# Optimization experiments

Hardware: AMD Instinct MI355X
Metric: run time of the kernel (lower is better)

Reference implementation:

```python
import jax, jax.numpy as jnp
import numpy as np

N_NODES = 100000
H_FEATS = 128
N_TRIPLETS = 500000


def setup_inputs() -> dict:
    key = jax.random.key(0)
    k_h, k_t, k_w1, k_b1, k_w2, k_b2 = jax.random.split(key, 6)
    h = jax.random.normal(k_h, (N_NODES, H_FEATS), dtype=jnp.float32)
    triplets = jax.random.randint(k_t, (N_TRIPLETS, 3), 0, N_NODES, dtype=jnp.int64)
    # nn.Linear weights: [out, in]
    W1_w = jax.random.normal(k_w1, (H_FEATS, 3 * H_FEATS), dtype=jnp.float32) * 0.05
    W1_b = jax.random.normal(k_b1, (H_FEATS,), dtype=jnp.float32) * 0.05
    W2_w = jax.random.normal(k_w2, (2, H_FEATS), dtype=jnp.float32) * 0.05
    W2_b = jax.random.normal(k_b2, (2,), dtype=jnp.float32) * 0.05
    return {"h": h, "triplets": triplets, "W1_w": W1_w, "W1_b": W1_b,
            "W2_w": W2_w, "W2_b": W2_b}


def reference(h, triplets, W1_w, W1_b, W2_w, W2_b):
    # gather: [T, 3, H] -> [T, 3*H]
    T = triplets.shape[0]
    emb = h[triplets].reshape(T, 3 * H_FEATS)
    hid = jax.nn.relu(emb @ W1_w.T + W1_b)   # [T, H]
    out = hid @ W2_w.T + W2_b                # [T, 2]
    return out
```

## Files before the change

### kernel.cpp

```cpp
#include <hip/hip_runtime.h>

typedef __bf16 bf16x8 __attribute__((ext_vector_type(8)));
typedef float f32x4 __attribute__((ext_vector_type(4)));

__device__ __forceinline__ unsigned short f2bf(float x) {
  union { float f; unsigned int i; } u; u.f = x;
  return (unsigned short)((u.i + 0x7FFFu + ((u.i >> 16) & 1u)) >> 16);
}
__device__ __forceinline__ float bf2f(unsigned short b) {
  union { unsigned int i; float f; } u; u.i = ((unsigned int)b) << 16;
  return u.f;
}
__device__ __forceinline__ bf16x8 cvt8(float4 a, float4 b) {
  union { unsigned short u[8]; bf16x8 v; } r;
  r.u[0] = f2bf(a.x); r.u[1] = f2bf(a.y); r.u[2] = f2bf(a.z); r.u[3] = f2bf(a.w);
  r.u[4] = f2bf(b.x); r.u[5] = f2bf(b.y); r.u[6] = f2bf(b.z); r.u[7] = f2bf(b.w);
  return r.v;
}

__global__ void pack_w1_kernel(const float* __restrict__ W1w, uint4* __restrict__ wp) {
  int fid = blockIdx.x * 256 + threadIdx.x;
  int kk = fid / 1536;
  int rem = fid - kk * 1536;
  int nf = rem >> 6;
  int ln = rem & 63;
  int ng = nf * 16 + (ln & 15);
  int c = ng & 127;
  int jp = ng >> 7;
  int k0 = kk * 32 + (ln >> 4) * 8;
  const float* src = W1w + (size_t)c * 384 + jp * 128 + k0;
  float4 a = *(const float4*)src;
  float4 b = *(const float4*)(src + 4);
  union { unsigned short u[8]; uint4 v; } r;
  r.u[0] = f2bf(a.x); r.u[1] = f2bf(a.y); r.u[2] = f2bf(a.z); r.u[3] = f2bf(a.w);
  r.u[4] = f2bf(b.x); r.u[5] = f2bf(b.y); r.u[6] = f2bf(b.z); r.u[7] = f2bf(b.w);
  wp[fid] = r.v;
}

#define OT_STRIDE 200
__global__ __launch_bounds__(512, 6) void phaseA_kernel(
    const float* __restrict__ h, const uint4* __restrict__ wp,
    unsigned short* __restrict__ P, int Nn, int ntiles) {
  __shared__ uint4 wl[48 * 64];
  const int tid = threadIdx.x;
  const int b = blockIdx.x;
  const int xcd = b & 7;
  const int j = b >> 3;
  const int cs = j & 1;
  const int tile = (j >> 1) * 8 + xcd;
  if (tile >= ntiles) return;

  for (int i = tid; i < 48 * 64; i += 512) {
    int fr = i >> 6;
    int ln = i & 63;
    int kk = fr / 12, nfl = fr - kk * 12;
    wl[i] = wp[(kk * 24 + cs * 12 + nfl) * 64 + ln];
  }
  __syncthreads();

  const int lane = tid & 63;
  const int wv = tid >> 6;
  const int rg = wv >> 1;
  const int cg = wv & 1;
  const int l15 = lane & 15;
  const int lg = lane >> 4;

  const int mb = tile * 64 + rg * 16;
  int arow = mb + l15;
  if (arow >= Nn) arow = Nn - 1;
  const float* ap = h + (size_t)arow * 128 + lg * 8;

  f32x4 acc[6];
#pragma unroll
  for (int nf = 0; nf < 6; nf++) acc[nf] = (f32x4){0.f, 0.f, 0.f, 0.f};

#pragma unroll
  for (int kk = 0; kk < 4; kk++) {
    bf16x8 af = cvt8(*(const float4*)(ap + kk * 32), *(const float4*)(ap + kk * 32 + 4));
#pragma unroll
    for (int nf = 0; nf < 6; nf++) {
      bf16x8 bf = __builtin_bit_cast(bf16x8, wl[(kk * 12 + cg * 6 + nf) * 64 + lane]);
      acc[nf] = __builtin_amdgcn_mfma_f32_16x16x32_bf16(af, bf, acc[nf], 0, 0, 0);
    }
  }

  __syncthreads();
  unsigned short* ot = (unsigned short*)wl;
#pragma unroll
  for (int nf = 0; nf < 6; nf++)
#pragma unroll
    for (int r = 0; r < 4; r++)
      ot[(rg * 16 + lg * 4 + r) * OT_STRIDE + cg * 96 + nf * 16 + l15] =
          f2bf(acc[nf][r]);
  __syncthreads();

  const int r0 = tile * 64;
  if (r0 + 64 <= Nn) {
#pragma unroll
    for (int pass = 0; pass < 3; pass++) {
      int i = pass * 512 + tid;
      int row = i / 24, c = i - row * 24;
      uint4 v = *(const uint4*)&ot[row * OT_STRIDE + c * 8];
      *(uint4*)(P + (size_t)(r0 + row) * 384 + cs * 192 + c * 8) = v;
    }
  } else {
    for (int i = tid; i < 64 * 24; i += 512) {
      int row = i / 24, c = i - row * 24;
      if (r0 + row < Nn) {
        uint4 v = *(const uint4*)&ot[row * OT_STRIDE + c * 8];
        *(uint4*)(P + (size_t)(r0 + row) * 384 + cs * 192 + c * 8) = v;
      }
    }
  }
}

__global__ __launch_bounds__(256) void phaseB_kernel(
    const unsigned short* __restrict__ P, const int* __restrict__ trip,
    const float* __restrict__ b1, const float* __restrict__ W2w,
    const float* __restrict__ b2, float* __restrict__ out, int T) {
  constexpr int U = 5;
  const int gtid = blockIdx.x * 256 + threadIdx.x;
  const int g0 = gtid >> 4;
  const int c8 = threadIdx.x & 15;
  const int ng = (gridDim.x * 256) >> 4;
  const int c0 = c8 * 8;

  float4 b1a = *(const float4*)(b1 + c0), b1b = *(const float4*)(b1 + c0 + 4);
  float4 w0a = *(const float4*)(W2w + c0), w0b = *(const float4*)(W2w + c0 + 4);
  float4 w1a = *(const float4*)(W2w + 128 + c0), w1b = *(const float4*)(W2w + 128 + c0 + 4);
  const float bb0 = b2[0], bb1 = b2[1];
  float b1r[8] = {b1a.x, b1a.y, b1a.z, b1a.w, b1b.x, b1b.y, b1b.z, b1b.w};
  float w20[8] = {w0a.x, w0a.y, w0a.z, w0a.w, w0b.x, w0b.y, w0b.z, w0b.w};
  float w21[8] = {w1a.x, w1a.y, w1a.z, w1a.w, w1b.x, w1b.y, w1b.z, w1b.w};

  for (int t = g0; t < T; t += U * ng) {
    int tc[U];
    bool hv[U];
#pragma unroll
    for (int u = 0; u < U; u++) {
      int tt = t + u * ng;
      hv[u] = tt < T;
      tc[u] = hv[u] ? tt : t;
    }
    union { uint4 v; unsigned short u[8]; } va[U][3];
#pragma unroll
    for (int u = 0; u < U; u++) {
      int i0 = trip[3 * tc[u]], i1 = trip[3 * tc[u] + 1], i2 = trip[3 * tc[u] + 2];
      va[u][0].v = *((const uint4*)(P + (size_t)i0 * 384) + c8);
      va[u][1].v = *((const uint4*)(P + (size_t)i1 * 384 + 128) + c8);
      va[u][2].v = *((const uint4*)(P + (size_t)i2 * 384 + 256) + c8);
    }
    float p0[U], p1[U];
#pragma unroll
    for (int u = 0; u < U; u++) {
      p0[u] = 0.f; p1[u] = 0.f;
#pragma unroll
      for (int j = 0; j < 8; j++) {
        float s = bf2f(va[u][0].u[j]) + bf2f(va[u][1].u[j]) + bf2f(va[u][2].u[j]) + b1r[j];
        s = fmaxf(s, 0.f);
        p0[u] = fmaf(s, w20[j], p0[u]);
        p1[u] = fmaf(s, w21[j], p1[u]);
      }
    }
#pragma unroll
    for (int d = 1; d < 16; d <<= 1) {
#pragma unroll
      for (int u = 0; u < U; u++) {
        p0[u] += __shfl_xor(p0[u], d);
        p1[u] += __shfl_xor(p1[u], d);
      }
    }
    if (c8 == 0) {
#pragma unroll
      for (int u = 0; u < U; u++) {
        if (hv[u]) {
          float2 o;
          o.x = p0[u] + bb0;
          o.y = p1[u] + bb1;
          *(float2*)(out + (size_t)(t + u * ng) * 2) = o;
        }
      }
    }
  }
}

__global__ __launch_bounds__(512, 2) void fused_fallback(
    const float* __restrict__ Hsrc, const int* __restrict__ trip,
    const float* __restrict__ W1w, const float* __restrict__ b1,
    const float* __restrict__ W2w, const float* __restrict__ b2,
    float* __restrict__ out, int T) {
  extern __shared__ unsigned short w1p[];
  const int tid = threadIdx.x;
  for (int f = tid; f < 6144; f += 512) {
    int kk = f >> 9; int nf = (f >> 6) & 7; int ln = f & 63;
    int row = nf * 16 + (ln & 15); int k0 = kk * 32 + (ln >> 4) * 8;
    const float* src = W1w + row * 384 + k0;
    float4 a = *(const float4*)src; float4 b = *(const float4*)(src + 4);
    union { unsigned short u[8]; uint4 v; } r;
    r.u[0] = f2bf(a.x); r.u[1] = f2bf(a.y); r.u[2] = f2bf(a.z); r.u[3] = f2bf(a.w);
    r.u[4] = f2bf(b.x); r.u[5] = f2bf(b.y); r.u[6] = f2bf(b.z); r.u[7] = f2bf(b.w);
    *(uint4*)&w1p[f * 8] = r.v;
  }
  __syncthreads();
  const int lane = tid & 63, wv = tid >> 6, l15 = lane & 15, lg = lane >> 4;
  float b1r[8], w20[8], w21[8];
#pragma unroll
  for (int nf = 0; nf < 8; nf++) {
    int c = nf * 16 + l15;
    b1r[nf] = b1[c]; w20[nf] = W2w[c]; w21[nf] = W2w[128 + c];
  }
  const float bb0 = b2[0], bb1 = b2[1];
  const int ntiles = (T + 511) >> 9;
  for (int tile = blockIdx.x; tile < ntiles; tile += gridDim.x) {
    const int base = tile * 512 + wv * 64;
    f32x4 acc[4][8];
#pragma unroll
    for (int m = 0; m < 4; m++)
#pragma unroll
      for (int nf = 0; nf < 8; nf++) acc[m][nf] = (f32x4){0.f, 0.f, 0.f, 0.f};
    int off[4][3];
#pragma unroll
    for (int m = 0; m < 4; m++) {
      int row = base + m * 16 + l15;
      int rc = row < T ? row : T - 1;
      off[m][0] = trip[rc * 3]; off[m][1] = trip[rc * 3 + 1]; off[m][2] = trip[rc * 3 + 2];
    }
#pragma unroll
    for (int part = 0; part < 3; part++)
#pragma unroll
      for (int kq = 0; kq < 4; kq++) {
        const int kk = part * 4 + kq;
        bf16x8 af[4];
#pragma unroll
        for (int m = 0; m < 4; m++) {
          const float* p = Hsrc + ((size_t)off[m][part] << 7) + kq * 32 + lg * 8;
          af[m] = cvt8(*(const float4*)p, *(const float4*)(p + 4));
        }
#pragma unroll
        for (int nf = 0; nf < 8; nf++) {
          bf16x8 bf = __builtin_bit_cast(bf16x8,
              *(const uint4*)&w1p[(size_t)(kk * 512 + nf * 64 + lane) * 8]);
#pragma unroll
          for (int m = 0; m < 4; m++)
            acc[m][nf] = __builtin_amdgcn_mfma_f32_16x16x32_bf16(af[m], bf, acc[m][nf], 0, 0, 0);
        }
      }
#pragma unroll
    for (int m = 0; m < 4; m++) {
      float p0[4] = {0, 0, 0, 0}, p1[4] = {0, 0, 0, 0};
#pragma unroll
      for (int nf = 0; nf < 8; nf++)
#pragma unroll
        for (int r = 0; r < 4; r++) {
          float hv = fmaxf(acc[m][nf][r] + b1r[nf], 0.f);
          p0[r] = fmaf(hv, w20[nf], p0[r]);
          p1[r] = fmaf(hv, w21[nf], p1[r]);
        }
#pragma unroll
      for (int d = 1; d < 16; d <<= 1)
#pragma unroll
        for (int r = 0; r < 4; r++) {
          p0[r] += __shfl_xor(p0[r], d);
          p1[r] += __shfl_xor(p1[r], d);
        }
#pragma unroll
      for (int r = 0; r < 4; r++)
        if (l15 == r) {
          int row = base + m * 16 + lg * 4 + r;
          if (row < T) {
            float2 o; o.x = p0[r] + bb0; o.y = p1[r] + bb1;
            *(float2*)(out + (size_t)row * 2) = o;
          }
        }
    }
  }
}

extern "C" void kernel_launch(void* const* d_in, const int* in_sizes, int n_in,
                              void* d_out, int out_size, void* d_ws, size_t ws_size,
                              hipStream_t stream) {
  const float* h = (const float*)d_in[0];
  const int* trip = (const int*)d_in[1];
  const float* W1w = (const float*)d_in[2];
  const float* b1 = (const float*)d_in[3];
  const float* W2w = (const float*)d_in[4];
  const float* b2 = (const float*)d_in[5];
  float* out = (float*)d_out;

  const int Nn = in_sizes[0] / 128;
  const int T = in_sizes[1] / 3;
  const size_t pbytes = (size_t)Nn * 384 * 2;
  const size_t need = pbytes + 6144 * 16;

  if (ws_size >= need) {
    unsigned short* P = (unsigned short*)d_ws;
    uint4* wp = (uint4*)((char*)d_ws + pbytes);
    pack_w1_kernel<<<24, 256, 0, stream>>>(W1w, wp);
    const int ntiles = (Nn + 63) >> 6;
    const int ntp = ((ntiles + 7) >> 3) << 3;
    phaseA_kernel<<<ntp * 2, 512, 0, stream>>>(h, wp, P, Nn, ntiles);
    phaseB_kernel<<<2048, 256, 0, stream>>>(P, trip, b1, W2w, b2, out, T);
  } else {
    fused_fallback<<<256, 512, 6144 * 16, stream>>>(h, trip, W1w, b1, W2w, b2, out, T);
  }
}
```

Before: 102.3 us.

## Split phase-A weight columns into three slices and process two row tiles per block

Phase A now divides the 384 projected output columns into three 128-column slices instead of two 192-column halves. Each block loads one 32KB weight slice into LDS and reuses it across two 64-row tiles of h. Output staging moves to a separate LDS buffer with a smaller stride. This amortizes the weight load over more rows and cuts per-block LDS and registers, but each h row is now read three times instead of twice, and the grid layout changes.

```diff
diff --git a/kernel.cpp b/kernel.cpp
--- a/kernel.cpp
+++ b/kernel.cpp
@@ -37,24 +37,24 @@
   wp[fid] = r.v;
 }
 
-#define OT_STRIDE 200
+#define OT_STRIDE 144
 __global__ __launch_bounds__(512, 6) void phaseA_kernel(
     const float* __restrict__ h, const uint4* __restrict__ wp,
     unsigned short* __restrict__ P, int Nn, int ntiles) {
-  __shared__ uint4 wl[48 * 64];
+  __shared__ uint4 wl[2048];
+  __shared__ unsigned short ot[64 * OT_STRIDE];
   const int tid = threadIdx.x;
   const int b = blockIdx.x;
   const int xcd = b & 7;
   const int j = b >> 3;
-  const int cs = j & 1;
-  const int tile = (j >> 1) * 8 + xcd;
-  if (tile >= ntiles) return;
-
-  for (int i = tid; i < 48 * 64; i += 512) {
-    int fr = i >> 6;
-    int ln = i & 63;
-    int kk = fr / 12, nfl = fr - kk * 12;
-    wl[i] = wp[(kk * 24 + cs * 12 + nfl) * 64 + ln];
+  const int slice = j % 3;
+  const int sg = j / 3;
+  const int super = sg * 8 + xcd;
+
+  for (int i = tid; i < 2048; i += 512) {
+    int fr = i >> 6, ln = i & 63;
+    int kk = fr >> 3, nfs = fr & 7;
+    wl[i] = wp[(kk * 24 + slice * 8 + nfs) * 64 + ln];
   }
   __syncthreads();
 
@@ -65,52 +65,56 @@
   const int l15 = lane & 15;
   const int lg = lane >> 4;
 
-  const int mb = tile * 64 + rg * 16;
-  int arow = mb + l15;
-  if (arow >= Nn) arow = Nn - 1;
-  const float* ap = h + (size_t)arow * 128 + lg * 8;
-
-  f32x4 acc[6];
-#pragma unroll
-  for (int nf = 0; nf < 6; nf++) acc[nf] = (f32x4){0.f, 0.f, 0.f, 0.f};
-
-#pragma unroll
-  for (int kk = 0; kk < 4; kk++) {
-    bf16x8 af = cvt8(*(const float4*)(ap + kk * 32), *(const float4*)(ap + kk * 32 + 4));
-#pragma unroll
-    for (int nf = 0; nf < 6; nf++) {
-      bf16x8 bf = __builtin_bit_cast(bf16x8, wl[(kk * 12 + cg * 6 + nf) * 64 + lane]);
-      acc[nf] = __builtin_amdgcn_mfma_f32_16x16x32_bf16(af, bf, acc[nf], 0, 0, 0);
-    }
-  }
-
-  __syncthreads();
-  unsigned short* ot = (unsigned short*)wl;
-#pragma unroll
-  for (int nf = 0; nf < 6; nf++)
-#pragma unroll
-    for (int r = 0; r < 4; r++)
-      ot[(rg * 16 + lg * 4 + r) * OT_STRIDE + cg * 96 + nf * 16 + l15] =
-          f2bf(acc[nf][r]);
-  __syncthreads();
-
-  const int r0 = tile * 64;
-  if (r0 + 64 <= Nn) {
-#pragma unroll
-    for (int pass = 0; pass < 3; pass++) {
-      int i = pass * 512 + tid;
-      int row = i / 24, c = i - row * 24;
-      uint4 v = *(const uint4*)&ot[row * OT_STRIDE + c * 8];
-      *(uint4*)(P + (size_t)(r0 + row) * 384 + cs * 192 + c * 8) = v;
-    }
-  } else {
-    for (int i = tid; i < 64 * 24; i += 512) {
-      int row = i / 24, c = i - row * 24;
-      if (r0 + row < Nn) {
+#pragma unroll
+  for (int tt = 0; tt < 2; tt++) {
+    const int tile = super * 2 + tt;
+    if (tile >= ntiles) break;
+    const int mb = tile * 64 + rg * 16;
+    int arow = mb + l15;
+    if (arow >= Nn) arow = Nn - 1;
+    const float* ap = h + (size_t)arow * 128 + lg * 8;
+
+    f32x4 acc[4];
+#pragma unroll
+    for (int nf = 0; nf < 4; nf++) acc[nf] = (f32x4){0.f, 0.f, 0.f, 0.f};
+
+#pragma unroll
+    for (int kk = 0; kk < 4; kk++) {
+      bf16x8 af = cvt8(*(const float4*)(ap + kk * 32), *(const float4*)(ap + kk * 32 + 4));
+#pragma unroll
+      for (int nf = 0; nf < 4; nf++) {
+        bf16x8 bf = __builtin_bit_cast(bf16x8, wl[(kk * 8 + cg * 4 + nf) * 64 + lane]);
+        acc[nf] = __builtin_amdgcn_mfma_f32_16x16x32_bf16(af, bf, acc[nf], 0, 0, 0);
+      }
+    }
+
+#pragma unroll
+    for (int nf = 0; nf < 4; nf++)
+#pragma unroll
+      for (int r = 0; r < 4; r++)
+        ot[(rg * 16 + lg * 4 + r) * OT_STRIDE + cg * 64 + nf * 16 + l15] =
+            f2bf(acc[nf][r]);
+    __syncthreads();
+
+    const int r0 = tile * 64;
+    if (r0 + 64 <= Nn) {
+#pragma unroll
+      for (int pass = 0; pass < 2; pass++) {
+        int i = pass * 512 + tid;
+        int row = i >> 4, c = i & 15;
         uint4 v = *(const uint4*)&ot[row * OT_STRIDE + c * 8];
-        *(uint4*)(P + (size_t)(r0 + row) * 384 + cs * 192 + c * 8) = v;
-      }
-    }
+        *(uint4*)(P + (size_t)(r0 + row) * 384 + slice * 128 + c * 8) = v;
+      }
+    } else {
+      for (int i = tid; i < 1024; i += 512) {
+        int row = i >> 4, c = i & 15;
+        if (r0 + row < Nn) {
+          uint4 v = *(const uint4*)&ot[row * OT_STRIDE + c * 8];
+          *(uint4*)(P + (size_t)(r0 + row) * 384 + slice * 128 + c * 8) = v;
+        }
+      }
+    }
+    __syncthreads();
   }
 }
 
@@ -297,8 +301,9 @@
     uint4* wp = (uint4*)((char*)d_ws + pbytes);
     pack_w1_kernel<<<24, 256, 0, stream>>>(W1w, wp);
     const int ntiles = (Nn + 63) >> 6;
-    const int ntp = ((ntiles + 7) >> 3) << 3;
-    phaseA_kernel<<<ntp * 2, 512, 0, stream>>>(h, wp, P, Nn, ntiles);
+    const int supers = (ntiles + 1) >> 1;
+    const int sgs = (supers + 7) >> 3;
+    phaseA_kernel<<<sgs * 8 * 3, 512, 0, stream>>>(h, wp, P, Nn, ntiles);
     phaseB_kernel<<<2048, 256, 0, stream>>>(P, trip, b1, W2w, b2, out, T);
   } else {
     fused_fallback<<<256, 512, 6144 * 16, stream>>>(h, trip, W1w, b1, W2w, b2, out, T);
```

Measured after the change: 111.5 us. 9.1% more time.
